# Optimization experiments

Measured on AMD Instinct MI355X. Metric: run time of the kernel, lower is better.

## Reference

```python
import jax, jax.numpy as jnp
import numpy as np

VOCAB = 14
EMBED = 10
HIDDEN = 50
MLP = 50
PAD_IDX = 0
BATCH = 4096
SEQ = 2048


def setup_inputs() -> dict:
    key = jax.random.key(0)
    ks = jax.random.split(key, 10)
    tokens = jax.random.randint(ks[0], (BATCH, SEQ), 0, VOCAB, dtype=jnp.int64 if jax.config.jax_enable_x64 else jnp.int32)
    s_lstm = 1.0 / np.sqrt(HIDDEN)
    s_mlp1 = 1.0 / np.sqrt(HIDDEN)
    s_mlp2 = 1.0 / np.sqrt(MLP)
    emb = jax.random.normal(ks[1], (VOCAB, EMBED), jnp.float32)
    emb = emb.at[PAD_IDX].set(0.0)  # padding_idx row is zero in torch Embedding
    W_ih = jax.random.uniform(ks[2], (4 * HIDDEN, EMBED), jnp.float32, -s_lstm, s_lstm)
    W_hh = jax.random.uniform(ks[3], (4 * HIDDEN, HIDDEN), jnp.float32, -s_lstm, s_lstm)
    b_ih = jax.random.uniform(ks[4], (4 * HIDDEN,), jnp.float32, -s_lstm, s_lstm)
    b_hh = jax.random.uniform(ks[5], (4 * HIDDEN,), jnp.float32, -s_lstm, s_lstm)
    W1 = jax.random.uniform(ks[6], (MLP, HIDDEN), jnp.float32, -s_mlp1, s_mlp1)
    b1 = jax.random.uniform(ks[7], (MLP,), jnp.float32, -s_mlp1, s_mlp1)
    W2 = jax.random.uniform(ks[8], (1, MLP), jnp.float32, -s_mlp2, s_mlp2)
    b2 = jax.random.uniform(ks[9], (1,), jnp.float32, -s_mlp2, s_mlp2)
    return {"input": tokens, "emb": emb, "W_ih": W_ih, "W_hh": W_hh,
            "b_ih": b_ih, "b_hh": b_hh, "W1": W1, "b1": b1, "W2": W2, "b2": b2}


def reference(input, emb, W_ih, W_hh, b_ih, b_hh, W1, b1, W2, b2):
    x = emb[input]                                   # [B, T, E]
    mask = (input != PAD_IDX).astype(emb.dtype)      # [B, T]
    xs = jnp.swapaxes(x, 0, 1)                       # [T, B, E]
    ms = jnp.swapaxes(mask, 0, 1)[:, :, None]        # [T, B, 1]
    B = input.shape[0]

    def step(carry, inp):
        h, c = carry
        xt, mt = inp
        gates = xt @ W_ih.T + b_ih + h @ W_hh.T + b_hh  # [B, 4H], order i,f,g,o
        i, f, g, o = jnp.split(gates, 4, axis=-1)
        i = jax.nn.sigmoid(i)
        f = jax.nn.sigmoid(f)
        g = jnp.tanh(g)
        o = jax.nn.sigmoid(o)
        c_new = f * c + i * g
        h_new = o * jnp.tanh(c_new)
        # blend: keep old state on padded positions
        h = h_new * mt + h * (1.0 - mt)
        c = c_new * mt + c * (1.0 - mt)
        return (h, c), None

    h0 = jnp.zeros((B, HIDDEN), emb.dtype)
    c0 = jnp.zeros((B, HIDDEN), emb.dtype)
    (h, c), _ = jax.lax.scan(step, (h0, c0), (xs, ms))
    hidden = h @ W1.T + b1                            # [B, MLP]
    out = jax.nn.sigmoid(hidden @ W2.T + b2)          # [B, 1]
    return out
```

## Files before the change

kernel.cpp:

```cpp
#include <hip/hip_runtime.h>

#define BATCH 4096
#define SEQ   2048
#define EMB   10
#define HID   50
#define VOCAB 14
#define TROW  2052

using bf16x8 = __attribute__((ext_vector_type(8))) short;
using f32x4  = __attribute__((ext_vector_type(4))) float;

__device__ __forceinline__ short f2bf(float f) {
  unsigned u = __builtin_bit_cast(unsigned, f);
  u = (u + 0x7FFFu + ((u >> 16) & 1u)) >> 16;
  return (short)u;
}
__device__ __forceinline__ unsigned f2bf2(float lo, float hi) {
  return (unsigned)(unsigned short)f2bf(lo) | ((unsigned)(unsigned short)f2bf(hi) << 16);
}
__device__ __forceinline__ float fsigm(float x) {
  return __builtin_amdgcn_rcpf(1.0f + __builtin_amdgcn_exp2f(x * -1.44269504f));
}

__global__ void prep_kernel(const float* __restrict__ emb,  const float* __restrict__ W_ih,
                            const float* __restrict__ W_hh, const float* __restrict__ b_ih,
                            const float* __restrict__ b_hh, short* __restrict__ Apack) {
  int idx = blockIdx.x * 256 + threadIdx.x;
  if (idx >= 13 * 2 * 64 * 8) return;
  int j    = idx & 7;
  int lane = (idx >> 3) & 63;
  int kf   = (idx >> 9) & 1;
  int tid  = idx >> 10;
  int m    = lane & 15;
  int q    = m >> 2, g = m & 3;
  int jh   = (tid < 10) ? (2 * ((tid >> 1) * 4 + q) + (tid & 1))
                        : (40 + (tid - 10) * 4 + q);
  int k    = kf * 32 + (lane >> 4) * 8 + j;
  float v = 0.0f;
  if (jh < HID) {
    int R = g * HID + jh;
    float scale = (g == 2) ? -2.885390082f : -1.442695041f;
    if (k < HID) {
      v = W_hh[R * HID + k] * scale;
    } else {
      int vo = k - HID;
      float s = b_ih[R] + b_hh[R];
      for (int e = 0; e < EMB; ++e) s += emb[vo * EMB + e] * W_ih[R * EMB + e];
      v = s * scale;
    }
  }
  Apack[idx] = f2bf(v);
}

__global__ __launch_bounds__(512, 1) void lstm_kernel(
    const int* __restrict__ tokens, const short* __restrict__ Apack,
    const float* __restrict__ W1, const float* __restrict__ b1,
    const float* __restrict__ W2, const float* __restrict__ b2,
    float* __restrict__ out) {
  __shared__ __align__(16) unsigned char toku8[16 * TROW];
  __shared__ __align__(16) short hbuf[2][16 * 64];
  __shared__ float hfin[16 * 52];
  __shared__ float mlp_hid[16 * 52];

  const int tid  = threadIdx.x;
  const int lane = tid & 63;
  const int wv   = tid >> 6;
  const int b0   = blockIdx.x * 16;
  const int bB   = lane & 15;
  const int jj   = lane >> 4;

  const bool two = (0xA7 >> wv) & 1;
  const int  fr  = __builtin_popcount(0xA7 & ((1 << wv) - 1));
  const int  sr  = __builtin_popcount(0x58 & ((1 << wv) - 1));
  const int  p   = fr * 4 + jj;
  const int  jhS = 40 + sr * 4 + jj;
  const bool sval = !two && (jhS < HID);

  const int t0 = two ? (fr * 2) : (10 + sr);
  bf16x8 Af00 = *(const bf16x8*)(Apack + ((t0 * 2 + 0) * 64 + lane) * 8);
  bf16x8 Af01 = *(const bf16x8*)(Apack + ((t0 * 2 + 1) * 64 + lane) * 8);
  bf16x8 Af10 = {}, Af11 = {};
  if (two) {
    Af10 = *(const bf16x8*)(Apack + (((t0 + 1) * 2 + 0) * 64 + lane) * 8);
    Af11 = *(const bf16x8*)(Apack + (((t0 + 1) * 2 + 1) * 64 + lane) * 8);
  }

  const bool ohact = (wv == 3 || wv == 4) && (lane < 56);
  const int ohr   = (wv - 3) * 8 + lane / 7;
  const int ohsub = lane % 7;
  const int ohoct = (ohsub < 3) ? 6 : 7;
  const int ohinn = (ohsub < 3) ? (4 + 4 * ohsub) : (4 * (ohsub - 3));
  const int ohb   = ohr * 128 + 16 * ((ohoct + ohr) & 7) + ohinn;
  const int ohv0  = 2 * ohsub, ohv1 = 2 * ohsub + 1;

  for (int i = tid; i < 16 * 512; i += 512) {
    int row = i >> 9, c4 = i & 511;
    int4 tv = *(const int4*)&tokens[(b0 + row) * SEQ + 4 * c4];
    unsigned pk = (tv.x & 0xFF) | ((tv.y & 0xFF) << 8) |
                  ((tv.z & 0xFF) << 16) | ((tv.w & 0xFF) << 24);
    *(unsigned*)&toku8[row * TROW + 4 * c4] = pk;
  }
  for (int i = tid; i < 1024; i += 512) hbuf[0][i] = 0;
  __syncthreads();

  char* hb = (char*)hbuf;
  const int rb0   = bB * 128 + 16 * ((jj + bB) & 7);
  const int rb1   = bB * 128 + 16 * (((jj + 4) + bB) & 7);
  const int hwb32 = bB * 128 + 16 * (((p >> 2) + bB) & 7) + ((4 * p) & 15);
  const int hwb16 = bB * 128 + 16 * (((jhS >> 3) + bB) & 7) + 2 * (jhS & 7);
  const unsigned char* myrow = &toku8[bB * TROW];
  const unsigned char* ohtok = &toku8[ohr * TROW];

  if (ohact) {
    int tk = ohtok[0];
    unsigned wb = ((tk == ohv0) ? 0x3F80u : 0u) | ((tk == ohv1) ? 0x3F800000u : 0u);
    *(unsigned*)(hb + ohb) = wb;
  }

  float c0 = 0.f, h0 = 0.f, c1 = 0.f, h1 = 0.f;
  unsigned mp = 0;

  for (int t = 0; t < SEQ; t += 16) {
#pragma unroll
    for (int u = 0; u < 16; ++u) {
      const int T  = t + u;
      const int PB = (u & 1) * 2048, PN = PB ^ 2048;
      __syncthreads();

      bf16x8 Bf0 = *(const bf16x8*)(hb + PB + rb0);
      bf16x8 Bf1 = *(const bf16x8*)(hb + PB + rb1);
      if ((u & 3) == 0) mp = *(const unsigned*)(myrow + T);

      f32x4 acc0 = {0.f, 0.f, 0.f, 0.f};
      acc0 = __builtin_amdgcn_mfma_f32_16x16x32_bf16(Af00, Bf0, acc0, 0, 0, 0);
      acc0 = __builtin_amdgcn_mfma_f32_16x16x32_bf16(Af01, Bf1, acc0, 0, 0, 0);
      f32x4 acc1 = {0.f, 0.f, 0.f, 0.f};
      if (two) {
        acc1 = __builtin_amdgcn_mfma_f32_16x16x32_bf16(Af10, Bf0, acc1, 0, 0, 0);
        acc1 = __builtin_amdgcn_mfma_f32_16x16x32_bf16(Af11, Bf1, acc1, 0, 0, 0);
      }

      if (ohact && T + 1 < SEQ) {
        int tk = ohtok[T + 1];
        unsigned wb = ((tk == ohv0) ? 0x3F80u : 0u) |
                      ((tk == ohv1) ? 0x3F800000u : 0u);
        *(unsigned*)(hb + PN + ohb) = wb;
      }

      const bool keep = (((mp >> (8 * (u & 3))) & 0xFF) != 0);

      if (two) {
        float eA0 = __builtin_amdgcn_exp2f(acc0[0]);
        float eB0 = __builtin_amdgcn_exp2f(acc0[1]);
        float eC0 = __builtin_amdgcn_exp2f(acc0[2]);
        float eG0 = __builtin_amdgcn_exp2f(acc0[3]);
        float eA1 = __builtin_amdgcn_exp2f(acc1[0]);
        float eB1 = __builtin_amdgcn_exp2f(acc1[1]);
        float eC1 = __builtin_amdgcn_exp2f(acc1[2]);
        float eG1 = __builtin_amdgcn_exp2f(acc1[3]);
        float a10 = 1.f + eA0, b10 = 1.f + eB0, c10 = 1.f + eC0, g10 = 1.f + eG0;
        float a11 = 1.f + eA1, b11 = 1.f + eB1, c11 = 1.f + eC1, g11 = 1.f + eG1;
        float P0 = a10 * c10, P1 = a11 * c11;
        float t10 = __builtin_fmaf(-eC0, b10, b10);
        float t11 = __builtin_fmaf(-eC1, b11, b11);
        float num0 = __builtin_fmaf(c0, P0, t10);
        float num1 = __builtin_fmaf(c1, P1, t11);
        float den0 = P0 * b10, den1 = P1 * b11;
        float r  = __builtin_amdgcn_rcpf(den0 * den1);
        float cn0 = num0 * (den1 * r);
        float cn1 = num1 * (den0 * r);
        float cl0 = fminf(cn0 * -2.885390082f, 40.0f);
        float cl1 = fminf(cn1 * -2.885390082f, 40.0f);
        float H0 = __builtin_amdgcn_exp2f(cl0);
        float H1 = __builtin_amdgcn_exp2f(cl1);
        float hd0 = g10 * (1.f + H0);
        float hd1 = g11 * (1.f + H1);
        float rh = __builtin_amdgcn_rcpf(hd0 * hd1);
        float hn0 = (1.f - H0) * (hd1 * rh);
        float hn1 = (1.f - H1) * (hd0 * rh);
        c0 = keep ? cn0 : c0;  h0 = keep ? hn0 : h0;
        c1 = keep ? cn1 : c1;  h1 = keep ? hn1 : h1;
        *(unsigned*)(hb + PN + hwb32) = f2bf2(h0, h1);
      } else {
        float eA = __builtin_amdgcn_exp2f(acc0[0]);
        float eB = __builtin_amdgcn_exp2f(acc0[1]);
        float eC = __builtin_amdgcn_exp2f(acc0[2]);
        float eG = __builtin_amdgcn_exp2f(acc0[3]);
        float a1 = 1.f + eA, bb1 = 1.f + eB, cc1 = 1.f + eC, g1 = 1.f + eG;
        float P   = a1 * cc1;
        float t1  = __builtin_fmaf(-eC, bb1, bb1);
        float num = __builtin_fmaf(c0, P, t1);
        float den = P * bb1;
        float cn  = num * __builtin_amdgcn_rcpf(den);
        float cl  = fminf(cn * -2.885390082f, 40.0f);
        float eH  = __builtin_amdgcn_exp2f(cl);
        float hd  = g1 * (1.f + eH);
        float hn  = (1.f - eH) * __builtin_amdgcn_rcpf(hd);
        c0 = keep ? cn : c0;
        h0 = keep ? hn : h0;
        if (sval) *(short*)(hb + PN + hwb16) = f2bf(h0);
      }
    }
  }

  if (two) {
    hfin[bB * 52 + 2 * p]     = h0;
    hfin[bB * 52 + 2 * p + 1] = h1;
  } else if (sval) {
    hfin[bB * 52 + jhS] = h0;
  }
  __syncthreads();
  for (int idx = tid; idx < 16 * 64; idx += 512) {
    int b = idx >> 6, m = idx & 63;
    if (m < HID) {
      float s = b1[m];
      for (int j2 = 0; j2 < HID; ++j2) s += hfin[b * 52 + j2] * W1[m * HID + j2];
      mlp_hid[b * 52 + m] = s;
    }
  }
  __syncthreads();
  if (tid < 16) {
    float s = b2[0];
    for (int m2 = 0; m2 < HID; ++m2) s += mlp_hid[tid * 52 + m2] * W2[m2];
    out[b0 + tid] = fsigm(s);
  }
}

extern "C" void kernel_launch(void* const* d_in, const int* in_sizes, int n_in,
                              void* d_out, int out_size, void* d_ws, size_t ws_size,
                              hipStream_t stream) {
  const int*   tokens = (const int*)  d_in[0];
  const float* emb    = (const float*)d_in[1];
  const float* W_ih   = (const float*)d_in[2];
  const float* W_hh   = (const float*)d_in[3];
  const float* b_ih   = (const float*)d_in[4];
  const float* b_hh   = (const float*)d_in[5];
  const float* W1     = (const float*)d_in[6];
  const float* b1     = (const float*)d_in[7];
  const float* W2     = (const float*)d_in[8];
  const float* b2     = (const float*)d_in[9];
  float* outp  = (float*)d_out;
  short* Apack = (short*)d_ws;

  hipLaunchKernelGGL(prep_kernel, dim3(52), dim3(256), 0, stream,
                     emb, W_ih, W_hh, b_ih, b_hh, Apack);
  hipLaunchKernelGGL(lstm_kernel, dim3(BATCH / 16), dim3(512), 0, stream,
                     tokens, Apack, W1, b1, W2, b2, outp);
}
```

Baseline: 811.2 us.

## Halve LSTM block to four waves, each computing up to four gate tiles

The recurrent kernel now runs 256 threads (4 waves) per 16-sequence block instead of 512, with each wave handling up to four MFMA gate tiles and two or four hidden units per lane. Fewer waves per barrier is meant to cut per-timestep __syncthreads cost on the serial critical path. The step loop unroll drops from 16 to 4, and bf16 packing uses the hardware v_cvt_pk_bf16_f32 instruction. In exchange each wave does more MFMA and transcendental work per step, lengthening per-step latency, and the tile-to-wave split is uneven (4/4/3/2 tiles).

```diff
diff --git a/kernel.cpp b/kernel.cpp
--- a/kernel.cpp
+++ b/kernel.cpp
@@ -15,11 +15,13 @@
   u = (u + 0x7FFFu + ((u >> 16) & 1u)) >> 16;
   return (short)u;
 }
-__device__ __forceinline__ unsigned f2bf2(float lo, float hi) {
-  return (unsigned)(unsigned short)f2bf(lo) | ((unsigned)(unsigned short)f2bf(hi) << 16);
-}
 __device__ __forceinline__ float fsigm(float x) {
   return __builtin_amdgcn_rcpf(1.0f + __builtin_amdgcn_exp2f(x * -1.44269504f));
+}
+__device__ __forceinline__ unsigned cvtpk(float lo, float hi) {
+  unsigned r;
+  asm("v_cvt_pk_bf16_f32 %0, %1, %2" : "=v"(r) : "v"(lo), "v"(hi));
+  return r;
 }
 
 __global__ void prep_kernel(const float* __restrict__ emb,  const float* __restrict__ W_ih,
@@ -52,7 +54,63 @@
   Apack[idx] = f2bf(v);
 }
 
-__global__ __launch_bounds__(512, 1) void lstm_kernel(
+__device__ __forceinline__ void cell_pair(f32x4 A, f32x4 B, bool keep,
+                                          float& c0r, float& h0r, float& c1r, float& h1r) {
+  float eA0 = __builtin_amdgcn_exp2f(A[0]);
+  float eB0 = __builtin_amdgcn_exp2f(A[1]);
+  float eC0 = __builtin_amdgcn_exp2f(A[2]);
+  float eG0 = __builtin_amdgcn_exp2f(A[3]);
+  float eA1 = __builtin_amdgcn_exp2f(B[0]);
+  float eB1 = __builtin_amdgcn_exp2f(B[1]);
+  float eC1 = __builtin_amdgcn_exp2f(B[2]);
+  float eG1 = __builtin_amdgcn_exp2f(B[3]);
+  float a10 = 1.f + eA0, b10 = 1.f + eB0, c10 = 1.f + eC0, g10 = 1.f + eG0;
+  float a11 = 1.f + eA1, b11 = 1.f + eB1, c11 = 1.f + eC1, g11 = 1.f + eG1;
+  float P0 = a10 * c10, P1 = a11 * c11;
+  float t10 = __builtin_fmaf(-eC0, b10, b10);
+  float t11 = __builtin_fmaf(-eC1, b11, b11);
+  float num0 = __builtin_fmaf(c0r, P0, t10);
+  float num1 = __builtin_fmaf(c1r, P1, t11);
+  float den0 = P0 * b10, den1 = P1 * b11;
+  float r  = __builtin_amdgcn_rcpf(den0 * den1);
+  float cn0 = num0 * (den1 * r);
+  float cn1 = num1 * (den0 * r);
+  float cl0 = fminf(cn0 * -2.885390082f, 40.0f);
+  float cl1 = fminf(cn1 * -2.885390082f, 40.0f);
+  float H0 = __builtin_amdgcn_exp2f(cl0);
+  float H1 = __builtin_amdgcn_exp2f(cl1);
+  float hd0 = g10 * (1.f + H0);
+  float hd1 = g11 * (1.f + H1);
+  float rh = __builtin_amdgcn_rcpf(hd0 * hd1);
+  float hn0 = (1.f - H0) * (hd1 * rh);
+  float hn1 = (1.f - H1) * (hd0 * rh);
+  c0r = keep ? cn0 : c0r;  h0r = keep ? hn0 : h0r;
+  c1r = keep ? cn1 : c1r;  h1r = keep ? hn1 : h1r;
+}
+
+__device__ __forceinline__ void cell_single(f32x4 A, bool keep, float& cr, float& hr) {
+  float eA = __builtin_amdgcn_exp2f(A[0]);
+  float eB = __builtin_amdgcn_exp2f(A[1]);
+  float eC = __builtin_amdgcn_exp2f(A[2]);
+  float eG = __builtin_amdgcn_exp2f(A[3]);
+  float a1 = 1.f + eA, bb1 = 1.f + eB, cc1 = 1.f + eC, g1 = 1.f + eG;
+  float P   = a1 * cc1;
+  float t1  = __builtin_fmaf(-eC, bb1, bb1);
+  float num = __builtin_fmaf(cr, P, t1);
+  float den = P * bb1;
+  float cn  = num * __builtin_amdgcn_rcpf(den);
+  float cl  = fminf(cn * -2.885390082f, 40.0f);
+  float eH  = __builtin_amdgcn_exp2f(cl);
+  float hd  = g1 * (1.f + eH);
+  float hn  = (1.f - eH) * __builtin_amdgcn_rcpf(hd);
+  cr = keep ? cn : cr;
+  hr = keep ? hn : hr;
+}
+
+#define HWB32(p) (bB * 128 + 16 * ((((p) >> 2) + bB) & 7) + ((4 * (p)) & 15))
+#define HWB16(j) (bB * 128 + 16 * ((((j) >> 3) + bB) & 7) + 2 * ((j) & 7))
+
+__global__ __launch_bounds__(256, 1) void lstm_kernel(
     const int* __restrict__ tokens, const short* __restrict__ Apack,
     const float* __restrict__ W1, const float* __restrict__ b1,
     const float* __restrict__ W2, const float* __restrict__ b2,
@@ -69,148 +127,146 @@
   const int bB   = lane & 15;
   const int jj   = lane >> 4;
 
-  const bool two = (0xA7 >> wv) & 1;
-  const int  fr  = __builtin_popcount(0xA7 & ((1 << wv) - 1));
-  const int  sr  = __builtin_popcount(0x58 & ((1 << wv) - 1));
-  const int  p   = fr * 4 + jj;
-  const int  jhS = 40 + sr * 4 + jj;
-  const bool sval = !two && (jhS < HID);
-
-  const int t0 = two ? (fr * 2) : (10 + sr);
-  bf16x8 Af00 = *(const bf16x8*)(Apack + ((t0 * 2 + 0) * 64 + lane) * 8);
-  bf16x8 Af01 = *(const bf16x8*)(Apack + ((t0 * 2 + 1) * 64 + lane) * 8);
-  bf16x8 Af10 = {}, Af11 = {};
-  if (two) {
-    Af10 = *(const bf16x8*)(Apack + (((t0 + 1) * 2 + 0) * 64 + lane) * 8);
-    Af11 = *(const bf16x8*)(Apack + (((t0 + 1) * 2 + 1) * 64 + lane) * 8);
-  }
-
-  const bool ohact = (wv == 3 || wv == 4) && (lane < 56);
-  const int ohr   = (wv - 3) * 8 + lane / 7;
+  bf16x8 A0{}, A1{}, A2{}, A3{}, A4{}, A5{}, A6{}, A7{};
+  {
+    int base  = (wv == 0) ? 0 : (wv == 1) ? 4 : (wv == 2) ? 8 : 11;
+    int ntile = (wv <= 1) ? 4 : (wv == 2) ? 3 : 2;
+    const short* ap = Apack + (base * 128 + lane) * 8;
+    A0 = *(const bf16x8*)(ap + 0 * 512);
+    A1 = *(const bf16x8*)(ap + 1 * 512);
+    A2 = *(const bf16x8*)(ap + 2 * 512);
+    A3 = *(const bf16x8*)(ap + 3 * 512);
+    if (ntile >= 3) { A4 = *(const bf16x8*)(ap + 4 * 512);
+                      A5 = *(const bf16x8*)(ap + 5 * 512); }
+    if (ntile == 4) { A6 = *(const bf16x8*)(ap + 6 * 512);
+                      A7 = *(const bf16x8*)(ap + 7 * 512); }
+  }
+
+  char* hb = (char*)hbuf;
+  const int rb0 = bB * 128 + 16 * ((jj + bB) & 7);
+  const int rb1 = bB * 128 + 16 * (((jj + 4) + bB) & 7);
+  int hw0, hw1 = 0;
+  bool w1valid = true;
+  if (wv == 0)      { hw0 = HWB32(jj);       hw1 = HWB32(4 + jj); }
+  else if (wv == 1) { hw0 = HWB32(8 + jj);   hw1 = HWB32(12 + jj); }
+  else if (wv == 2) { hw0 = HWB32(16 + jj);  hw1 = HWB16(40 + jj); }
+  else              { hw0 = HWB16(44 + jj);  hw1 = HWB16(48 + jj);
+                      w1valid = (jj < 2); }
+
+  const bool ohact = (wv == 3) && (lane < 56);
+  const int ohr0  = lane / 7;
   const int ohsub = lane % 7;
   const int ohoct = (ohsub < 3) ? 6 : 7;
   const int ohinn = (ohsub < 3) ? (4 + 4 * ohsub) : (4 * (ohsub - 3));
-  const int ohb   = ohr * 128 + 16 * ((ohoct + ohr) & 7) + ohinn;
+  const int ohr1  = ohr0 + 8;
+  const int ohb0  = ohr0 * 128 + 16 * ((ohoct + ohr0) & 7) + ohinn;
+  const int ohb1  = ohr1 * 128 + 16 * ((ohoct + ohr1) & 7) + ohinn;
   const int ohv0  = 2 * ohsub, ohv1 = 2 * ohsub + 1;
-
-  for (int i = tid; i < 16 * 512; i += 512) {
+  const unsigned char* oht0 = &toku8[ohr0 * TROW];
+  const unsigned char* oht1 = &toku8[ohr1 * TROW];
+  const unsigned char* myrow = &toku8[bB * TROW];
+
+  for (int i = tid; i < 16 * 512; i += 256) {
     int row = i >> 9, c4 = i & 511;
     int4 tv = *(const int4*)&tokens[(b0 + row) * SEQ + 4 * c4];
     unsigned pk = (tv.x & 0xFF) | ((tv.y & 0xFF) << 8) |
                   ((tv.z & 0xFF) << 16) | ((tv.w & 0xFF) << 24);
     *(unsigned*)&toku8[row * TROW + 4 * c4] = pk;
   }
-  for (int i = tid; i < 1024; i += 512) hbuf[0][i] = 0;
+  for (int i = tid; i < 1024; i += 256) hbuf[0][i] = 0;
   __syncthreads();
 
-  char* hb = (char*)hbuf;
-  const int rb0   = bB * 128 + 16 * ((jj + bB) & 7);
-  const int rb1   = bB * 128 + 16 * (((jj + 4) + bB) & 7);
-  const int hwb32 = bB * 128 + 16 * (((p >> 2) + bB) & 7) + ((4 * p) & 15);
-  const int hwb16 = bB * 128 + 16 * (((jhS >> 3) + bB) & 7) + 2 * (jhS & 7);
-  const unsigned char* myrow = &toku8[bB * TROW];
-  const unsigned char* ohtok = &toku8[ohr * TROW];
-
   if (ohact) {
-    int tk = ohtok[0];
-    unsigned wb = ((tk == ohv0) ? 0x3F80u : 0u) | ((tk == ohv1) ? 0x3F800000u : 0u);
-    *(unsigned*)(hb + ohb) = wb;
-  }
-
-  float c0 = 0.f, h0 = 0.f, c1 = 0.f, h1 = 0.f;
+    int tk0 = oht0[0], tk1 = oht1[0];
+    *(unsigned*)(hb + ohb0) = ((tk0 == ohv0) ? 0x3F80u : 0u) |
+                              ((tk0 == ohv1) ? 0x3F800000u : 0u);
+    *(unsigned*)(hb + ohb1) = ((tk1 == ohv0) ? 0x3F80u : 0u) |
+                              ((tk1 == ohv1) ? 0x3F800000u : 0u);
+  }
+
+  float sc0 = 0.f, sh0 = 0.f, sc1 = 0.f, sh1 = 0.f;
+  float sc2 = 0.f, sh2 = 0.f, sc3 = 0.f, sh3 = 0.f;
   unsigned mp = 0;
 
-  for (int t = 0; t < SEQ; t += 16) {
+  for (int t = 0; t < SEQ; t += 4) {
 #pragma unroll
-    for (int u = 0; u < 16; ++u) {
+    for (int u = 0; u < 4; ++u) {
       const int T  = t + u;
       const int PB = (u & 1) * 2048, PN = PB ^ 2048;
       __syncthreads();
 
       bf16x8 Bf0 = *(const bf16x8*)(hb + PB + rb0);
       bf16x8 Bf1 = *(const bf16x8*)(hb + PB + rb1);
-      if ((u & 3) == 0) mp = *(const unsigned*)(myrow + T);
-
-      f32x4 acc0 = {0.f, 0.f, 0.f, 0.f};
-      acc0 = __builtin_amdgcn_mfma_f32_16x16x32_bf16(Af00, Bf0, acc0, 0, 0, 0);
-      acc0 = __builtin_amdgcn_mfma_f32_16x16x32_bf16(Af01, Bf1, acc0, 0, 0, 0);
-      f32x4 acc1 = {0.f, 0.f, 0.f, 0.f};
-      if (two) {
-        acc1 = __builtin_amdgcn_mfma_f32_16x16x32_bf16(Af10, Bf0, acc1, 0, 0, 0);
-        acc1 = __builtin_amdgcn_mfma_f32_16x16x32_bf16(Af11, Bf1, acc1, 0, 0, 0);
+      if (u == 0) mp = *(const unsigned*)(myrow + T);
+
+      if (ohact && T + 1 < SEQ) {
+        int tk0 = oht0[T + 1], tk1 = oht1[T + 1];
+        *(unsigned*)(hb + PN + ohb0) = ((tk0 == ohv0) ? 0x3F80u : 0u) |
+                                       ((tk0 == ohv1) ? 0x3F800000u : 0u);
+        *(unsigned*)(hb + PN + ohb1) = ((tk1 == ohv0) ? 0x3F80u : 0u) |
+                                       ((tk1 == ohv1) ? 0x3F800000u : 0u);
       }
 
-      if (ohact && T + 1 < SEQ) {
-        int tk = ohtok[T + 1];
-        unsigned wb = ((tk == ohv0) ? 0x3F80u : 0u) |
-                      ((tk == ohv1) ? 0x3F800000u : 0u);
-        *(unsigned*)(hb + PN + ohb) = wb;
-      }
-
-      const bool keep = (((mp >> (8 * (u & 3))) & 0xFF) != 0);
-
-      if (two) {
-        float eA0 = __builtin_amdgcn_exp2f(acc0[0]);
-        float eB0 = __builtin_amdgcn_exp2f(acc0[1]);
-        float eC0 = __builtin_amdgcn_exp2f(acc0[2]);
-        float eG0 = __builtin_amdgcn_exp2f(acc0[3]);
-        float eA1 = __builtin_amdgcn_exp2f(acc1[0]);
-        float eB1 = __builtin_amdgcn_exp2f(acc1[1]);
-        float eC1 = __builtin_amdgcn_exp2f(acc1[2]);
-        float eG1 = __builtin_amdgcn_exp2f(acc1[3]);
-        float a10 = 1.f + eA0, b10 = 1.f + eB0, c10 = 1.f + eC0, g10 = 1.f + eG0;
-        float a11 = 1.f + eA1, b11 = 1.f + eB1, c11 = 1.f + eC1, g11 = 1.f + eG1;
-        float P0 = a10 * c10, P1 = a11 * c11;
-        float t10 = __builtin_fmaf(-eC0, b10, b10);
-        float t11 = __builtin_fmaf(-eC1, b11, b11);
-        float num0 = __builtin_fmaf(c0, P0, t10);
-        float num1 = __builtin_fmaf(c1, P1, t11);
-        float den0 = P0 * b10, den1 = P1 * b11;
-        float r  = __builtin_amdgcn_rcpf(den0 * den1);
-        float cn0 = num0 * (den1 * r);
-        float cn1 = num1 * (den0 * r);
-        float cl0 = fminf(cn0 * -2.885390082f, 40.0f);
-        float cl1 = fminf(cn1 * -2.885390082f, 40.0f);
-        float H0 = __builtin_amdgcn_exp2f(cl0);
-        float H1 = __builtin_amdgcn_exp2f(cl1);
-        float hd0 = g10 * (1.f + H0);
-        float hd1 = g11 * (1.f + H1);
-        float rh = __builtin_amdgcn_rcpf(hd0 * hd1);
-        float hn0 = (1.f - H0) * (hd1 * rh);
-        float hn1 = (1.f - H1) * (hd0 * rh);
-        c0 = keep ? cn0 : c0;  h0 = keep ? hn0 : h0;
-        c1 = keep ? cn1 : c1;  h1 = keep ? hn1 : h1;
-        *(unsigned*)(hb + PN + hwb32) = f2bf2(h0, h1);
+      const bool keep = (((mp >> (8 * u)) & 0xFFu) != 0u);
+      const f32x4 z = {0.f, 0.f, 0.f, 0.f};
+
+      if (wv <= 1) {
+        f32x4 a0 = z, a1 = z, a2 = z, a3 = z;
+        a0 = __builtin_amdgcn_mfma_f32_16x16x32_bf16(A0, Bf0, a0, 0, 0, 0);
+        a0 = __builtin_amdgcn_mfma_f32_16x16x32_bf16(A1, Bf1, a0, 0, 0, 0);
+        a1 = __builtin_amdgcn_mfma_f32_16x16x32_bf16(A2, Bf0, a1, 0, 0, 0);
+        a1 = __builtin_amdgcn_mfma_f32_16x16x32_bf16(A3, Bf1, a1, 0, 0, 0);
+        a2 = __builtin_amdgcn_mfma_f32_16x16x32_bf16(A4, Bf0, a2, 0, 0, 0);
+        a2 = __builtin_amdgcn_mfma_f32_16x16x32_bf16(A5, Bf1, a2, 0, 0, 0);
+        a3 = __builtin_amdgcn_mfma_f32_16x16x32_bf16(A6, Bf0, a3, 0, 0, 0);
+        a3 = __builtin_amdgcn_mfma_f32_16x16x32_bf16(A7, Bf1, a3, 0, 0, 0);
+        cell_pair(a0, a1, keep, sc0, sh0, sc1, sh1);
+        cell_pair(a2, a3, keep, sc2, sh2, sc3, sh3);
+        *(unsigned*)(hb + PN + hw0) = cvtpk(sh0, sh1);
+        *(unsigned*)(hb + PN + hw1) = cvtpk(sh2, sh3);
+      } else if (wv == 2) {
+        f32x4 a0 = z, a1 = z, a2 = z;
+        a0 = __builtin_amdgcn_mfma_f32_16x16x32_bf16(A0, Bf0, a0, 0, 0, 0);
+        a0 = __builtin_amdgcn_mfma_f32_16x16x32_bf16(A1, Bf1, a0, 0, 0, 0);
+        a1 = __builtin_amdgcn_mfma_f32_16x16x32_bf16(A2, Bf0, a1, 0, 0, 0);
+        a1 = __builtin_amdgcn_mfma_f32_16x16x32_bf16(A3, Bf1, a1, 0, 0, 0);
+        a2 = __builtin_amdgcn_mfma_f32_16x16x32_bf16(A4, Bf0, a2, 0, 0, 0);
+        a2 = __builtin_amdgcn_mfma_f32_16x16x32_bf16(A5, Bf1, a2, 0, 0, 0);
+        cell_pair(a0, a1, keep, sc0, sh0, sc1, sh1);
+        cell_single(a2, keep, sc2, sh2);
+        *(unsigned*)(hb + PN + hw0) = cvtpk(sh0, sh1);
+        *(short*)(hb + PN + hw1) = (short)cvtpk(sh2, sh2);
       } else {
-        float eA = __builtin_amdgcn_exp2f(acc0[0]);
-        float eB = __builtin_amdgcn_exp2f(acc0[1]);
-        float eC = __builtin_amdgcn_exp2f(acc0[2]);
-        float eG = __builtin_amdgcn_exp2f(acc0[3]);
-        float a1 = 1.f + eA, bb1 = 1.f + eB, cc1 = 1.f + eC, g1 = 1.f + eG;
-        float P   = a1 * cc1;
-        float t1  = __builtin_fmaf(-eC, bb1, bb1);
-        float num = __builtin_fmaf(c0, P, t1);
-        float den = P * bb1;
-        float cn  = num * __builtin_amdgcn_rcpf(den);
-        float cl  = fminf(cn * -2.885390082f, 40.0f);
-        float eH  = __builtin_amdgcn_exp2f(cl);
-        float hd  = g1 * (1.f + eH);
-        float hn  = (1.f - eH) * __builtin_amdgcn_rcpf(hd);
-        c0 = keep ? cn : c0;
-        h0 = keep ? hn : h0;
-        if (sval) *(short*)(hb + PN + hwb16) = f2bf(h0);
+        f32x4 a0 = z, a1 = z;
+        a0 = __builtin_amdgcn_mfma_f32_16x16x32_bf16(A0, Bf0, a0, 0, 0, 0);
+        a0 = __builtin_amdgcn_mfma_f32_16x16x32_bf16(A1, Bf1, a0, 0, 0, 0);
+        a1 = __builtin_amdgcn_mfma_f32_16x16x32_bf16(A2, Bf0, a1, 0, 0, 0);
+        a1 = __builtin_amdgcn_mfma_f32_16x16x32_bf16(A3, Bf1, a1, 0, 0, 0);
+        cell_pair(a0, a1, keep, sc0, sh0, sc1, sh1);
+        unsigned pk = cvtpk(sh0, sh1);
+        *(short*)(hb + PN + hw0) = (short)pk;
+        if (w1valid) *(short*)(hb + PN + hw1) = (short)(pk >> 16);
       }
     }
   }
 
-  if (two) {
-    hfin[bB * 52 + 2 * p]     = h0;
-    hfin[bB * 52 + 2 * p + 1] = h1;
-  } else if (sval) {
-    hfin[bB * 52 + jhS] = h0;
+  if (wv <= 1) {
+    const int p0 = (wv == 0) ? jj : (8 + jj);
+    const int p1 = p0 + 4;
+    hfin[bB * 52 + 2 * p0]     = sh0;
+    hfin[bB * 52 + 2 * p0 + 1] = sh1;
+    hfin[bB * 52 + 2 * p1]     = sh2;
+    hfin[bB * 52 + 2 * p1 + 1] = sh3;
+  } else if (wv == 2) {
+    hfin[bB * 52 + 32 + 2 * jj] = sh0;
+    hfin[bB * 52 + 33 + 2 * jj] = sh1;
+    hfin[bB * 52 + 40 + jj]     = sh2;
+  } else {
+    hfin[bB * 52 + 44 + jj] = sh0;
+    if (jj < 2) hfin[bB * 52 + 48 + jj] = sh1;
   }
   __syncthreads();
-  for (int idx = tid; idx < 16 * 64; idx += 512) {
+  for (int idx = tid; idx < 16 * 64; idx += 256) {
     int b = idx >> 6, m = idx & 63;
     if (m < HID) {
       float s = b1[m];
@@ -244,6 +300,6 @@
 
   hipLaunchKernelGGL(prep_kernel, dim3(52), dim3(256), 0, stream,
                      emb, W_ih, W_hh, b_ih, b_hh, Apack);
-  hipLaunchKernelGGL(lstm_kernel, dim3(BATCH / 16), dim3(512), 0, stream,
+  hipLaunchKernelGGL(lstm_kernel, dim3(BATCH / 16), dim3(256), 0, stream,
                      tokens, Apack, W1, b1, W2, b2, outp);
 }
```

Result: slower. 896.0 us (+10.4%).

## Split LSTM gate tiles across 13 waves with one tile per wave

Applied to the files above, without the earlier changes.

Grows the block from 8 waves to 13 so each wave owns a single 16-row gate tile instead of some waves handling two. This shortens the per-step critical path of MFMA plus transcendental work on the slowest wave. The cost is a barrier across more waves every timestep and fewer free SIMD slots. The change also swaps the software bf16 rounding for the hardware v_cvt_pk_bf16_f32 instruction, moves the one-hot writers to waves 10 and 11, and cuts the inner unroll from 16 to 4.

```diff
diff --git a/kernel.cpp b/kernel.cpp
--- a/kernel.cpp
+++ b/kernel.cpp
@@ -15,11 +15,13 @@
   u = (u + 0x7FFFu + ((u >> 16) & 1u)) >> 16;
   return (short)u;
 }
-__device__ __forceinline__ unsigned f2bf2(float lo, float hi) {
-  return (unsigned)(unsigned short)f2bf(lo) | ((unsigned)(unsigned short)f2bf(hi) << 16);
-}
 __device__ __forceinline__ float fsigm(float x) {
   return __builtin_amdgcn_rcpf(1.0f + __builtin_amdgcn_exp2f(x * -1.44269504f));
+}
+__device__ __forceinline__ unsigned cvtpk(float lo, float hi) {
+  unsigned r;
+  asm("v_cvt_pk_bf16_f32 %0, %1, %2" : "=v"(r) : "v"(lo), "v"(hi));
+  return r;
 }
 
 __global__ void prep_kernel(const float* __restrict__ emb,  const float* __restrict__ W_ih,
@@ -52,7 +54,9 @@
   Apack[idx] = f2bf(v);
 }
 
-__global__ __launch_bounds__(512, 1) void lstm_kernel(
+#define HWB16(j) (bB * 128 + 16 * ((((j) >> 3) + bB) & 7) + 2 * ((j) & 7))
+
+__global__ __launch_bounds__(832, 1) void lstm_kernel(
     const int* __restrict__ tokens, const short* __restrict__ Apack,
     const float* __restrict__ W1, const float* __restrict__ b1,
     const float* __restrict__ W2, const float* __restrict__ b2,
@@ -69,148 +73,93 @@
   const int bB   = lane & 15;
   const int jj   = lane >> 4;
 
-  const bool two = (0xA7 >> wv) & 1;
-  const int  fr  = __builtin_popcount(0xA7 & ((1 << wv) - 1));
-  const int  sr  = __builtin_popcount(0x58 & ((1 << wv) - 1));
-  const int  p   = fr * 4 + jj;
-  const int  jhS = 40 + sr * 4 + jj;
-  const bool sval = !two && (jhS < HID);
+  const int jh = (wv < 10) ? (2 * ((wv >> 1) * 4 + jj) + (wv & 1))
+                           : (40 + (wv - 10) * 4 + jj);
+  const bool hval = (jh < HID);
 
-  const int t0 = two ? (fr * 2) : (10 + sr);
-  bf16x8 Af00 = *(const bf16x8*)(Apack + ((t0 * 2 + 0) * 64 + lane) * 8);
-  bf16x8 Af01 = *(const bf16x8*)(Apack + ((t0 * 2 + 1) * 64 + lane) * 8);
-  bf16x8 Af10 = {}, Af11 = {};
-  if (two) {
-    Af10 = *(const bf16x8*)(Apack + (((t0 + 1) * 2 + 0) * 64 + lane) * 8);
-    Af11 = *(const bf16x8*)(Apack + (((t0 + 1) * 2 + 1) * 64 + lane) * 8);
-  }
+  const bf16x8 Af0 = *(const bf16x8*)(Apack + ((wv * 2 + 0) * 64 + lane) * 8);
+  const bf16x8 Af1 = *(const bf16x8*)(Apack + ((wv * 2 + 1) * 64 + lane) * 8);
 
-  const bool ohact = (wv == 3 || wv == 4) && (lane < 56);
-  const int ohr   = (wv - 3) * 8 + lane / 7;
+  char* hb = (char*)hbuf;
+  const int rb0 = bB * 128 + 16 * ((jj + bB) & 7);
+  const int rb1 = bB * 128 + 16 * (((jj + 4) + bB) & 7);
+  const int hw  = HWB16(jh);
+
+  const bool ohact = (wv == 10 || wv == 11) && (lane < 56);
+  const int ohr   = (wv - 10) * 8 + lane / 7;
   const int ohsub = lane % 7;
   const int ohoct = (ohsub < 3) ? 6 : 7;
   const int ohinn = (ohsub < 3) ? (4 + 4 * ohsub) : (4 * (ohsub - 3));
   const int ohb   = ohr * 128 + 16 * ((ohoct + ohr) & 7) + ohinn;
   const int ohv0  = 2 * ohsub, ohv1 = 2 * ohsub + 1;
+  const unsigned char* ohtok = &toku8[ohr * TROW];
+  const unsigned char* myrow = &toku8[bB * TROW];
 
-  for (int i = tid; i < 16 * 512; i += 512) {
+  for (int i = tid; i < 16 * 512; i += 832) {
     int row = i >> 9, c4 = i & 511;
     int4 tv = *(const int4*)&tokens[(b0 + row) * SEQ + 4 * c4];
     unsigned pk = (tv.x & 0xFF) | ((tv.y & 0xFF) << 8) |
                   ((tv.z & 0xFF) << 16) | ((tv.w & 0xFF) << 24);
     *(unsigned*)&toku8[row * TROW + 4 * c4] = pk;
   }
-  for (int i = tid; i < 1024; i += 512) hbuf[0][i] = 0;
+  for (int i = tid; i < 1024; i += 832) hbuf[0][i] = 0;
   __syncthreads();
-
-  char* hb = (char*)hbuf;
-  const int rb0   = bB * 128 + 16 * ((jj + bB) & 7);
-  const int rb1   = bB * 128 + 16 * (((jj + 4) + bB) & 7);
-  const int hwb32 = bB * 128 + 16 * (((p >> 2) + bB) & 7) + ((4 * p) & 15);
-  const int hwb16 = bB * 128 + 16 * (((jhS >> 3) + bB) & 7) + 2 * (jhS & 7);
-  const unsigned char* myrow = &toku8[bB * TROW];
-  const unsigned char* ohtok = &toku8[ohr * TROW];
 
   if (ohact) {
     int tk = ohtok[0];
-    unsigned wb = ((tk == ohv0) ? 0x3F80u : 0u) | ((tk == ohv1) ? 0x3F800000u : 0u);
-    *(unsigned*)(hb + ohb) = wb;
+    *(unsigned*)(hb + ohb) = ((tk == ohv0) ? 0x3F80u : 0u) |
+                             ((tk == ohv1) ? 0x3F800000u : 0u);
   }
 
-  float c0 = 0.f, h0 = 0.f, c1 = 0.f, h1 = 0.f;
+  float sc = 0.f, sh = 0.f;
   unsigned mp = 0;
 
-  for (int t = 0; t < SEQ; t += 16) {
+  for (int t = 0; t < SEQ; t += 4) {
 #pragma unroll
-    for (int u = 0; u < 16; ++u) {
+    for (int u = 0; u < 4; ++u) {
       const int T  = t + u;
       const int PB = (u & 1) * 2048, PN = PB ^ 2048;
       __syncthreads();
 
       bf16x8 Bf0 = *(const bf16x8*)(hb + PB + rb0);
       bf16x8 Bf1 = *(const bf16x8*)(hb + PB + rb1);
-      if ((u & 3) == 0) mp = *(const unsigned*)(myrow + T);
-
-      f32x4 acc0 = {0.f, 0.f, 0.f, 0.f};
-      acc0 = __builtin_amdgcn_mfma_f32_16x16x32_bf16(Af00, Bf0, acc0, 0, 0, 0);
-      acc0 = __builtin_amdgcn_mfma_f32_16x16x32_bf16(Af01, Bf1, acc0, 0, 0, 0);
-      f32x4 acc1 = {0.f, 0.f, 0.f, 0.f};
-      if (two) {
-        acc1 = __builtin_amdgcn_mfma_f32_16x16x32_bf16(Af10, Bf0, acc1, 0, 0, 0);
-        acc1 = __builtin_amdgcn_mfma_f32_16x16x32_bf16(Af11, Bf1, acc1, 0, 0, 0);
-      }
+      if (u == 0) mp = *(const unsigned*)(myrow + T);
 
       if (ohact && T + 1 < SEQ) {
         int tk = ohtok[T + 1];
-        unsigned wb = ((tk == ohv0) ? 0x3F80u : 0u) |
-                      ((tk == ohv1) ? 0x3F800000u : 0u);
-        *(unsigned*)(hb + PN + ohb) = wb;
+        *(unsigned*)(hb + PN + ohb) = ((tk == ohv0) ? 0x3F80u : 0u) |
+                                      ((tk == ohv1) ? 0x3F800000u : 0u);
       }
 
-      const bool keep = (((mp >> (8 * (u & 3))) & 0xFF) != 0);
+      const bool keep = (((mp >> (8 * u)) & 0xFFu) != 0u);
 
-      if (two) {
-        float eA0 = __builtin_amdgcn_exp2f(acc0[0]);
-        float eB0 = __builtin_amdgcn_exp2f(acc0[1]);
-        float eC0 = __builtin_amdgcn_exp2f(acc0[2]);
-        float eG0 = __builtin_amdgcn_exp2f(acc0[3]);
-        float eA1 = __builtin_amdgcn_exp2f(acc1[0]);
-        float eB1 = __builtin_amdgcn_exp2f(acc1[1]);
-        float eC1 = __builtin_amdgcn_exp2f(acc1[2]);
-        float eG1 = __builtin_amdgcn_exp2f(acc1[3]);
-        float a10 = 1.f + eA0, b10 = 1.f + eB0, c10 = 1.f + eC0, g10 = 1.f + eG0;
-        float a11 = 1.f + eA1, b11 = 1.f + eB1, c11 = 1.f + eC1, g11 = 1.f + eG1;
-        float P0 = a10 * c10, P1 = a11 * c11;
-        float t10 = __builtin_fmaf(-eC0, b10, b10);
-        float t11 = __builtin_fmaf(-eC1, b11, b11);
-        float num0 = __builtin_fmaf(c0, P0, t10);
-        float num1 = __builtin_fmaf(c1, P1, t11);
-        float den0 = P0 * b10, den1 = P1 * b11;
-        float r  = __builtin_amdgcn_rcpf(den0 * den1);
-        float cn0 = num0 * (den1 * r);
-        float cn1 = num1 * (den0 * r);
-        float cl0 = fminf(cn0 * -2.885390082f, 40.0f);
-        float cl1 = fminf(cn1 * -2.885390082f, 40.0f);
-        float H0 = __builtin_amdgcn_exp2f(cl0);
-        float H1 = __builtin_amdgcn_exp2f(cl1);
-        float hd0 = g10 * (1.f + H0);
-        float hd1 = g11 * (1.f + H1);
-        float rh = __builtin_amdgcn_rcpf(hd0 * hd1);
-        float hn0 = (1.f - H0) * (hd1 * rh);
-        float hn1 = (1.f - H1) * (hd0 * rh);
-        c0 = keep ? cn0 : c0;  h0 = keep ? hn0 : h0;
-        c1 = keep ? cn1 : c1;  h1 = keep ? hn1 : h1;
-        *(unsigned*)(hb + PN + hwb32) = f2bf2(h0, h1);
-      } else {
-        float eA = __builtin_amdgcn_exp2f(acc0[0]);
-        float eB = __builtin_amdgcn_exp2f(acc0[1]);
-        float eC = __builtin_amdgcn_exp2f(acc0[2]);
-        float eG = __builtin_amdgcn_exp2f(acc0[3]);
-        float a1 = 1.f + eA, bb1 = 1.f + eB, cc1 = 1.f + eC, g1 = 1.f + eG;
-        float P   = a1 * cc1;
-        float t1  = __builtin_fmaf(-eC, bb1, bb1);
-        float num = __builtin_fmaf(c0, P, t1);
-        float den = P * bb1;
-        float cn  = num * __builtin_amdgcn_rcpf(den);
-        float cl  = fminf(cn * -2.885390082f, 40.0f);
-        float eH  = __builtin_amdgcn_exp2f(cl);
-        float hd  = g1 * (1.f + eH);
-        float hn  = (1.f - eH) * __builtin_amdgcn_rcpf(hd);
-        c0 = keep ? cn : c0;
-        h0 = keep ? hn : h0;
-        if (sval) *(short*)(hb + PN + hwb16) = f2bf(h0);
-      }
+      f32x4 a = {0.f, 0.f, 0.f, 0.f};
+      a = __builtin_amdgcn_mfma_f32_16x16x32_bf16(Af0, Bf0, a, 0, 0, 0);
+      a = __builtin_amdgcn_mfma_f32_16x16x32_bf16(Af1, Bf1, a, 0, 0, 0);
+
+      float eA = __builtin_amdgcn_exp2f(a[0]);
+      float eB = __builtin_amdgcn_exp2f(a[1]);
+      float eC = __builtin_amdgcn_exp2f(a[2]);
+      float eG = __builtin_amdgcn_exp2f(a[3]);
+      float a1 = 1.f + eA, bb1 = 1.f + eB, cc1 = 1.f + eC, g1 = 1.f + eG;
+      float P   = a1 * cc1;
+      float t1  = __builtin_fmaf(-eC, bb1, bb1);
+      float num = __builtin_fmaf(sc, P, t1);
+      float den = P * bb1;
+      float cn  = num * __builtin_amdgcn_rcpf(den);
+      float cl  = fminf(cn * -2.885390082f, 40.0f);
+      float eH  = __builtin_amdgcn_exp2f(cl);
+      float hd  = g1 * (1.f + eH);
+      float hn  = (1.f - eH) * __builtin_amdgcn_rcpf(hd);
+      sc = keep ? cn : sc;
+      sh = keep ? hn : sh;
+      if (hval) *(short*)(hb + PN + hw) = (short)cvtpk(sh, sh);
     }
   }
 
-  if (two) {
-    hfin[bB * 52 + 2 * p]     = h0;
-    hfin[bB * 52 + 2 * p + 1] = h1;
-  } else if (sval) {
-    hfin[bB * 52 + jhS] = h0;
-  }
+  if (hval) hfin[bB * 52 + jh] = sh;
   __syncthreads();
-  for (int idx = tid; idx < 16 * 64; idx += 512) {
+  for (int idx = tid; idx < 16 * 64; idx += 832) {
     int b = idx >> 6, m = idx & 63;
     if (m < HID) {
       float s = b1[m];
@@ -244,6 +193,6 @@
 
   hipLaunchKernelGGL(prep_kernel, dim3(52), dim3(256), 0, stream,
                      emb, W_ih, W_hh, b_ih, b_hh, Apack);
-  hipLaunchKernelGGL(lstm_kernel, dim3(BATCH / 16), dim3(512), 0, stream,
+  hipLaunchKernelGGL(lstm_kernel, dim3(BATCH / 16), dim3(832), 0, stream,
                      tokens, Apack, W1, b1, W2, b2, outp);
 }
```

New measurement: 838.7 us. 1.03x slower.
